# Kernel optimization log

Hardware: AMD Instinct MI355X
Metric: run time of the kernel (lower is better)

The kernel has to match this reference:

```python
import jax, jax.numpy as jnp
import numpy as np

D_MODEL = 512
N_HEADS = 8
HEAD_DIM = D_MODEL // N_HEADS
ROPE_BASE = 10000.0


def _rope_cache(seq_len, dtype):
    half = HEAD_DIM // 2
    inv_freq = 1.0 / (ROPE_BASE ** (jnp.arange(half, dtype=dtype) / half))
    t = jnp.arange(seq_len, dtype=dtype)
    freqs = jnp.einsum('i,j->ij', t, inv_freq)            # [L, half]
    cos = jnp.repeat(jnp.cos(freqs), 2, axis=-1)          # [L, head_dim]
    sin = jnp.repeat(jnp.sin(freqs), 2, axis=-1)
    return cos[None, None], sin[None, None]               # [1,1,L,head_dim]


def _rotate_half(x):
    x_even = x[..., ::2]
    x_odd = x[..., 1::2]
    return jnp.stack([-x_odd, x_even], axis=-1).reshape(x.shape)


def setup_inputs() -> dict:
    key = jax.random.key(0)
    ks = jax.random.split(key, 10)
    B, Lq, Lkv, C = 2, 2048, 4096, D_MODEL
    s = 1.0 / np.sqrt(C)
    inp = {
        'q': jax.random.normal(ks[0], (B, Lq, C), jnp.float32),
        'kv': jax.random.normal(ks[1], (B, Lkv, C), jnp.float32),
        'Wq': jax.random.normal(ks[2], (C, C), jnp.float32) * s,
        'bq': jnp.zeros((C,), jnp.float32),
        'Wk': jax.random.normal(ks[3], (C, C), jnp.float32) * s,
        'bk': jnp.zeros((C,), jnp.float32),
        'Wv': jax.random.normal(ks[4], (C, C), jnp.float32) * s,
        'bv': jnp.zeros((C,), jnp.float32),
        'Wo': jax.random.normal(ks[5], (C, C), jnp.float32) * s,
        'bo': jnp.zeros((C,), jnp.float32),
    }
    return inp


def reference(q, kv, Wq, bq, Wk, bk, Wv, bv, Wo, bo):
    B, Lq, C = q.shape
    Lkv = kv.shape[1]
    H, Dh = N_HEADS, HEAD_DIM
    # projections (torch Linear: x @ W.T + b)
    qh = (q @ Wq.T + bq).reshape(B, Lq, H, Dh).transpose(0, 2, 1, 3)    # [B,H,Lq,Dh]
    kh = (kv @ Wk.T + bk).reshape(B, Lkv, H, Dh).transpose(0, 2, 1, 3)  # [B,H,Lkv,Dh]
    vh = (kv @ Wv.T + bv).reshape(B, Lkv, H, Dh).transpose(0, 2, 1, 3)
    # RoPE applied to K only
    cos, sin = _rope_cache(Lkv, kh.dtype)
    kh = kh * cos + _rotate_half(kh) * sin
    # manual softmax attention (full [B,H,Lq,Lkv] matrix, as in the source)
    scale = 1.0 / np.sqrt(Dh).astype(np.float32)
    attn = jnp.einsum('bhqd,bhkd->bhqk', qh, kh) * scale
    attn = jax.nn.softmax(attn, axis=-1)
    out = jnp.einsum('bhqk,bhkd->bhqd', attn, vh)
    out = out.transpose(0, 2, 1, 3).reshape(B, Lq, C)
    return out @ Wo.T + bo
```

## Files before the change

kernel.cpp:

```cpp
#include <hip/hip_runtime.h>
#include <math.h>

typedef _Float16 f16;
typedef __attribute__((ext_vector_type(8))) f16 f16x8;
typedef __attribute__((ext_vector_type(2))) f16 f16x2;
typedef __attribute__((ext_vector_type(4))) float f32x4;
typedef __attribute__((ext_vector_type(4))) int   i32x4;

__device__ __forceinline__ short f2h(float f) {
    return __builtin_bit_cast(short, (f16)f);
}
__device__ __forceinline__ float h2f(short s) {
    return (float)__builtin_bit_cast(f16, s);
}

__device__ __forceinline__ void gload16(const void* g, void* l) {
    __builtin_amdgcn_global_load_lds(
        (const __attribute__((address_space(1))) unsigned int*)g,
        (__attribute__((address_space(3))) unsigned int*)l, 16, 0, 0);
}

#define MFMA16(A, B, C) __builtin_amdgcn_mfma_f32_16x16x32_f16(A, B, C, 0, 0, 0)

__global__ __launch_bounds__(256) void convert_kernel(
    const float* __restrict__ q, const float* __restrict__ kv,
    const float* __restrict__ Wq, const float* __restrict__ Wk,
    const float* __restrict__ Wv, const float* __restrict__ Wo,
    short* __restrict__ cq, short* __restrict__ ckv,
    short* __restrict__ wq, short* __restrict__ wk,
    short* __restrict__ wv, short* __restrict__ wo)
{
    int g = blockIdx.x * 256 + threadIdx.x;
    const float* src; short* dst; int local;
    if      (g <  524288) { src = q;  dst = cq;  local = g; }
    else if (g < 1572864) { src = kv; dst = ckv; local = g -  524288; }
    else if (g < 1638400) { src = Wq; dst = wq;  local = g - 1572864; }
    else if (g < 1703936) { src = Wk; dst = wk;  local = g - 1638400; }
    else if (g < 1769472) { src = Wv; dst = wv;  local = g - 1703936; }
    else                  { src = Wo; dst = wo;  local = g - 1769472; }
    float4 v = *(const float4*)(src + (size_t)local * 4);
    short4 hv; short* hp = (short*)&hv;
    hp[0] = f2h(v.x); hp[1] = f2h(v.y); hp[2] = f2h(v.z); hp[3] = f2h(v.w);
    *(short4*)(dst + (size_t)local * 4) = hv;
}

template<int RT, int EP>
__device__ __forceinline__ void gemm_core(
    short* As, short* Bs,
    const short* __restrict__ X, const short* __restrict__ W,
    const float* __restrict__ bias, float scale,
    float* __restrict__ outF, short* __restrict__ outH,
    int m0, int n0)
{
    const int tid  = threadIdx.x;
    const int wave = tid >> 6, lane = tid & 63;
    const int quad = lane >> 4, col = lane & 15;
    const int wy = wave >> 1, wx = wave & 1;
    constexpr int MT = RT / 32;

    f32x4 acc[MT][4];
    #pragma unroll
    for (int i = 0; i < MT; ++i)
        #pragma unroll
        for (int j = 0; j < 4; ++j) acc[i][j] = (f32x4){0.f, 0.f, 0.f, 0.f};

    int aoff[MT], boff[4];
    #pragma unroll
    for (int t = 0; t < MT; ++t)
        aoff[t] = (wy * (RT / 2) + t * 16 + col) * 32 + quad * 8;
    #pragma unroll
    for (int t = 0; t < 4; ++t)
        boff[t] = (wx * 64 + t * 16 + col) * 32 + quad * 8;

    const short* Abase = X + (size_t)m0 * 512;
    const short* Bbase = W + (size_t)n0 * 512;

    for (int kb = 0; kb < 512; kb += 32) {
        __syncthreads();
        #pragma unroll
        for (int i = 0; i < RT / 64; ++i) {
            int p = i * 256 + tid;
            int r = p >> 2, qq = p & 3;
            gload16(Abase + (size_t)r * 512 + kb + qq * 8,
                    &As[(i * 256 + wave * 64) * 8]);
        }
        #pragma unroll
        for (int i = 0; i < 2; ++i) {
            int p = i * 256 + tid;
            int r = p >> 2, qq = p & 3;
            gload16(Bbase + (size_t)r * 512 + kb + qq * 8,
                    &Bs[(i * 256 + wave * 64) * 8]);
        }
        __syncthreads();

        f16x8 a[MT], b[4];
        #pragma unroll
        for (int t = 0; t < MT; ++t) a[t] = *(const f16x8*)&As[aoff[t]];
        #pragma unroll
        for (int t = 0; t < 4; ++t)  b[t] = *(const f16x8*)&Bs[boff[t]];
        #pragma unroll
        for (int tm = 0; tm < MT; ++tm)
            #pragma unroll
            for (int tn = 0; tn < 4; ++tn)
                acc[tm][tn] = MFMA16(a[tm], b[tn], acc[tm][tn]);
    }

    #pragma unroll
    for (int tn = 0; tn < 4; ++tn) {
        int ng = n0 + wx * 64 + tn * 16 + col;
        float bb = bias[ng];
        #pragma unroll
        for (int tm = 0; tm < MT; ++tm) {
            int mb = m0 + wy * (RT / 2) + tm * 16 + quad * 4;
            if constexpr (EP == 2) {
                int bb_ = mb >> 12, kvg = mb & 4095;
                int tile = kvg >> 7, kv128 = kvg & 127;
                int t01 = (kv128 >> 6) & 1, sv = (kv128 >> 4) & 3, qd = (kv128 >> 2) & 3;
                int hh = ng >> 6, dd = ng & 63, dt = dd >> 4, d15 = dd & 15;
                size_t base = ((((size_t)((bb_ * 8 + hh) * 32 + tile) * 16)
                               + sv * 4 + dt) * 64 + qd * 16 + d15) * 8 + t01 * 4;
                short4 s4; short* sp = (short*)&s4;
                #pragma unroll
                for (int r = 0; r < 4; ++r) sp[r] = f2h(acc[tm][tn][r] + bb);
                *(short4*)&outH[base] = s4;
            } else if constexpr (EP == 1) {
                #pragma unroll
                for (int r = 0; r < 4; ++r)
                    outH[(size_t)(mb + r) * 512 + ng] =
                        f2h((acc[tm][tn][r] + bb) * scale);
            } else {
                #pragma unroll
                for (int r = 0; r < 4; ++r)
                    outF[(size_t)(mb + r) * 512 + ng] = acc[tm][tn][r] + bb;
            }
        }
    }
}

__global__ __launch_bounds__(256) void fused_qkv_gemm_kernel(
    const short* __restrict__ cq, const short* __restrict__ ckv,
    const short* __restrict__ wq, const short* __restrict__ wk,
    const short* __restrict__ wv,
    const float* __restrict__ bq, const float* __restrict__ bk,
    const float* __restrict__ bv, float qscale,
    short* __restrict__ Qh, short* __restrict__ Kh, short* __restrict__ Vf)
{
    __shared__ short As[128 * 32], Bs[128 * 32];
    int bi = blockIdx.x;
    if (bi < 128) {
        gemm_core<128, 1>(As, Bs, cq, wq, bq, qscale, nullptr, Qh,
                          (bi >> 2) * 128, (bi & 3) * 128);
    } else if (bi < 384) {
        bi -= 128;
        gemm_core<128, 1>(As, Bs, ckv, wk, bk, 1.0f, nullptr, Kh,
                          (bi >> 2) * 128, (bi & 3) * 128);
    } else {
        bi -= 384;
        gemm_core<128, 2>(As, Bs, ckv, wv, bv, 1.0f, nullptr, Vf,
                          (bi >> 2) * 128, (bi & 3) * 128);
    }
}

__global__ __launch_bounds__(256) void gemm_o_kernel(
    const short* __restrict__ X, const short* __restrict__ W,
    const float* __restrict__ bias, float* __restrict__ outF)
{
    __shared__ short As[64 * 32], Bs[128 * 32];
    gemm_core<64, 0>(As, Bs, X, W, bias, 1.0f, outF, nullptr,
                     (int)(blockIdx.x >> 2) * 64, (int)(blockIdx.x & 3) * 128);
}

__global__ __launch_bounds__(256) void rope_kernel(short* __restrict__ Kh)
{
    __shared__ float2 tbl[4][32];
    const int t = threadIdx.x;
    const int g = blockIdx.x * 256 + t;
    if (t < 128) {
        int p = t >> 5, i = t & 31;
        int pos = (blockIdx.x * 4 + p) & 4095;
        float fr = expf((float)i * -0.28782313662425576f);
        float sv, cv;
        sincosf((float)pos * fr, &sv, &cv);
        tbl[p][i] = make_float2(cv, sv);
    }
    __syncthreads();

    int row = g >> 6;
    int c8  = (g & 63) * 8;
    size_t off = (size_t)row * 512 + c8;
    f16x8 hv = *(const f16x8*)&Kh[off];
    float x[8];
    #pragma unroll
    for (int j = 0; j < 8; ++j) x[j] = (float)hv[j];
    const int rl = row & 3;
    const int ib = (c8 & 63) >> 1;
    #pragma unroll
    for (int p = 0; p < 4; ++p) {
        float2 cs = tbl[rl][ib + p];
        float e = x[2 * p], o = x[2 * p + 1];
        x[2 * p]     = e * cs.x - o * cs.y;
        x[2 * p + 1] = o * cs.x + e * cs.y;
    }
    #pragma unroll
    for (int j = 0; j < 8; ++j) hv[j] = (f16)x[j];
    *(f16x8*)&Kh[off] = hv;
}

__global__ __launch_bounds__(256, 2) void attn_mfma_kernel(
    const short* __restrict__ Qh, const short* __restrict__ Kh,
    const short* __restrict__ Vfrag, short* __restrict__ AO)
{
    __shared__ char smem[65536];

    const int tid  = threadIdx.x;
    const int wave = tid >> 6;
    const int lane = tid & 63;
    const int quad = lane >> 4;
    const int l15  = lane & 15;

    const int bh = blockIdx.x & 15;
    const int qt = blockIdx.x >> 4;
    const int b  = bh >> 3, h = bh & 7;
    const int qb = qt * 64;

    f16x8 qf[4][2];
    #pragma unroll
    for (int tq = 0; tq < 4; ++tq)
        #pragma unroll
        for (int c = 0; c < 2; ++c)
            qf[tq][c] = *(const f16x8*)&Qh[((size_t)(b * 2048 + qb + tq * 16 + l15)) * 512
                                           + h * 64 + c * 32 + quad * 8];

    f32x4 o[4][4];
    f32x4 l4[4];
    #pragma unroll
    for (int i = 0; i < 4; ++i) {
        l4[i] = (f32x4){0.f, 0.f, 0.f, 0.f};
        #pragma unroll
        for (int j = 0; j < 4; ++j) o[i][j] = (f32x4){0.f, 0.f, 0.f, 0.f};
    }

    f16x8 vones;
    #pragma unroll
    for (int j = 0; j < 8; ++j) vones[j] = (f16)1.0f;

    const short* kp = Kh + ((size_t)(b * 4096 + wave * 16 + l15)) * 512
                      + h * 64 + quad * 8;
    const short* vbase = Vfrag + (size_t)(b * 8 + h) * 262144
                         + ((size_t)(wave * 4) * 64 + lane) * 8;

    short* sw = (short*)smem + wave * 8192;

#define STG(I2, P) {                                                         \
    const short* _src = kp + (size_t)(I2) * 65536;                           \
    short* _dst = sw + (P) * 2048;                                           \
    gload16(_src,              _dst);                                        \
    gload16(_src + 32,         _dst + 512);                                  \
    gload16(_src + 32768,      _dst + 1024);                                 \
    gload16(_src + 32768 + 32, _dst + 1536);                                 \
}

    STG(0, 0); STG(1, 1);
    f16x8 vf0[4], vf1[4];
    #pragma unroll
    for (int dt = 0; dt < 4; ++dt) vf0[dt] = *(const f16x8*)(vbase + dt * 512);

#define AITER(I, PAR, NPAR, VCUR, VNXT) {                                    \
           \
    asm volatile("s_waitcnt vmcnt(8)" ::: "memory");                         \
    const short* kb = sw + (PAR) * 2048;                                     \
    f16x8 k0[2], k1[2];                                                      \
    k0[0] = *(const f16x8*)(kb + lane * 8);                                  \
    k0[1] = *(const f16x8*)(kb + 512 + lane * 8);                            \
    k1[0] = *(const f16x8*)(kb + 1024 + lane * 8);                           \
    k1[1] = *(const f16x8*)(kb + 1536 + lane * 8);                           \
    {   const short* _vn = vbase + (size_t)((I) + 1) * 8192;                 \
        _Pragma("unroll")                                                    \
        for (int dt = 0; dt < 4; ++dt)                                       \
            VNXT[dt] = *(const f16x8*)(_vn + dt * 512); }                    \
    STG((I) + 2, NPAR);                                                      \
    f32x4 s0[4], s1[4];                                                      \
    _Pragma("unroll")                                                        \
    for (int t = 0; t < 4; ++t) {                                            \
        s0[t] = (f32x4){0.f, 0.f, 0.f, 0.f};                                 \
        s1[t] = (f32x4){0.f, 0.f, 0.f, 0.f};                                 \
    }                                                                        \
    __builtin_amdgcn_s_setprio(1);                                           \
    _Pragma("unroll")                                                        \
    for (int c = 0; c < 2; ++c)                                              \
        _Pragma("unroll")                                                    \
        for (int t = 0; t < 4; ++t) {                                        \
            s0[t] = MFMA16(k0[c], qf[t][c], s0[t]);                          \
            s1[t] = MFMA16(k1[c], qf[t][c], s1[t]);                          \
        }                                                                    \
    __builtin_amdgcn_s_setprio(0);                                           \
    _Pragma("unroll")                                                        \
    for (int t = 0; t < 4; ++t) {                                            \
        float e0 = exp2f(s0[t][0]), e1 = exp2f(s0[t][1]);                    \
        float e2 = exp2f(s0[t][2]), e3 = exp2f(s0[t][3]);                    \
        float e4 = exp2f(s1[t][0]), e5 = exp2f(s1[t][1]);                    \
        float e6 = exp2f(s1[t][2]), e7 = exp2f(s1[t][3]);                    \
        i32x4 pw;                                                            \
        pw.x = __builtin_bit_cast(int, __builtin_amdgcn_cvt_pkrtz(e0, e1));  \
        pw.y = __builtin_bit_cast(int, __builtin_amdgcn_cvt_pkrtz(e2, e3));  \
        pw.z = __builtin_bit_cast(int, __builtin_amdgcn_cvt_pkrtz(e4, e5));  \
        pw.w = __builtin_bit_cast(int, __builtin_amdgcn_cvt_pkrtz(e6, e7));  \
        f16x8 p8 = __builtin_bit_cast(f16x8, pw);                            \
        __builtin_amdgcn_s_setprio(1);                                       \
        _Pragma("unroll")                                                    \
        for (int dt = 0; dt < 4; ++dt)                                       \
            o[t][dt] = MFMA16(p8, VCUR[dt], o[t][dt]);                       \
        l4[t] = MFMA16(p8, vones, l4[t]);                                    \
        __builtin_amdgcn_s_setprio(0);                                       \
    }                                                                        \
}

    #pragma unroll 1
    for (int j = 0; j < 32; j += 4) {
        AITER(j + 0, 0, 2, vf0, vf1);
        AITER(j + 1, 1, 3, vf1, vf0);
        AITER(j + 2, 2, 0, vf0, vf1);
        AITER(j + 3, 3, 1, vf1, vf0);
    }
#undef AITER
#undef STG

    asm volatile("s_waitcnt vmcnt(0)" ::: "memory");
    __syncthreads();
    float* Opart = (float*)smem;
    float* Lpart = (float*)(smem + 33792);

    float inv_save[8];
    #pragma unroll
    for (int pass = 0; pass < 2; ++pass) {
        if (pass) __syncthreads();
        #pragma unroll
        for (int tq = 0; tq < 4; ++tq)
            #pragma unroll
            for (int dh = 0; dh < 2; ++dh) {
                int dt = pass * 2 + dh;
                #pragma unroll
                for (int r = 0; r < 4; ++r)
                    Opart[wave * (64 * 33) + (tq * 16 + quad * 4 + r) * 33 + dh * 16 + l15] = o[tq][dt][r];
            }
        if (pass == 0 && l15 == 0) {
            #pragma unroll
            for (int tq = 0; tq < 4; ++tq)
                #pragma unroll
                for (int r = 0; r < 4; ++r)
                    Lpart[wave * 64 + tq * 16 + quad * 4 + r] = l4[tq][r];
        }
        __syncthreads();
        #pragma unroll
        for (int r = 0; r < 8; ++r) {
            int qq = wave * 16 + r * 2 + (lane >> 5);
            int d  = lane & 31;
            float v = Opart[0 * (64 * 33) + qq * 33 + d] + Opart[1 * (64 * 33) + qq * 33 + d]
                    + Opart[2 * (64 * 33) + qq * 33 + d] + Opart[3 * (64 * 33) + qq * 33 + d];
            float inv;
            if (pass == 0) {
                float l = Lpart[qq] + Lpart[64 + qq] + Lpart[128 + qq] + Lpart[192 + qq];
                inv = 1.0f / l;
                inv_save[r] = inv;
            } else {
                inv = inv_save[r];
            }
            float val = v * inv;
            size_t oo = ((size_t)(b * 2048 + qb + qq)) * 512 + h * 64 + pass * 32 + d;
            AO[oo] = f2h(val);
        }
    }
}

extern "C" void kernel_launch(void* const* d_in, const int* in_sizes, int n_in,
                              void* d_out, int out_size, void* d_ws, size_t ws_size,
                              hipStream_t stream) {
    const float* q  = (const float*)d_in[0];
    const float* kv = (const float*)d_in[1];
    const float* Wq = (const float*)d_in[2];
    const float* bq = (const float*)d_in[3];
    const float* Wk = (const float*)d_in[4];
    const float* bk = (const float*)d_in[5];
    const float* Wv = (const float*)d_in[6];
    const float* bv = (const float*)d_in[7];
    const float* Wo = (const float*)d_in[8];
    const float* bo = (const float*)d_in[9];
    float* out = (float*)d_out;

    char* ws = (char*)d_ws;
    const size_t MB = 1024 * 1024;
    short* cq  = (short*)(ws + 0 * MB);
    short* ckv = (short*)(ws + 4 * MB);
    short* wq  = (short*)(ws + 12 * MB);
    short* wk  = wq + 262144;
    short* wv  = wk + 262144;
    short* wo  = wv + 262144;
    short* Qh  = (short*)(ws + 14 * MB);
    short* Kh  = (short*)(ws + 18 * MB);
    short* Vf  = (short*)(ws + 26 * MB);
    short* AO  = (short*)(ws + 34 * MB);

    const float qscale = 0.18033688011112043f;

    dim3 blk(256);
    convert_kernel<<<7168, blk, 0, stream>>>(
        q, kv, Wq, Wk, Wv, Wo, cq, ckv, wq, wk, wv, wo);

    fused_qkv_gemm_kernel<<<640, blk, 0, stream>>>(
        cq, ckv, wq, wk, wv, bq, bk, bv, qscale, Qh, Kh, Vf);

    rope_kernel<<<2048, blk, 0, stream>>>(Kh);

    attn_mfma_kernel<<<512, blk, 0, stream>>>(Qh, Kh, Vf, AO);

    gemm_o_kernel<<<256, blk, 0, stream>>>(AO, wo, bo, out);
}
```

Before: 175.7 us.

## Double-buffer GEMM LDS tiles and software-pipeline attention loop with register K/V

Result: faster. 166.1 us (-5.5%).

```diff
diff --git a/kernel.cpp b/kernel.cpp
--- a/kernel.cpp
+++ b/kernel.cpp
@@ -3,7 +3,6 @@
 
 typedef _Float16 f16;
 typedef __attribute__((ext_vector_type(8))) f16 f16x8;
-typedef __attribute__((ext_vector_type(2))) f16 f16x2;
 typedef __attribute__((ext_vector_type(4))) float f32x4;
 typedef __attribute__((ext_vector_type(4))) int   i32x4;
 
@@ -21,6 +20,7 @@
 }
 
 #define MFMA16(A, B, C) __builtin_amdgcn_mfma_f32_16x16x32_f16(A, B, C, 0, 0, 0)
+#define EXP2(x) __builtin_amdgcn_exp2f(x)
 
 __global__ __launch_bounds__(256) void convert_kernel(
     const float* __restrict__ q, const float* __restrict__ kv,
@@ -56,7 +56,8 @@
     const int wave = tid >> 6, lane = tid & 63;
     const int quad = lane >> 4, col = lane & 15;
     const int wy = wave >> 1, wx = wave & 1;
-    constexpr int MT = RT / 32;
+    constexpr int MT  = RT / 32;
+    constexpr int ASZ = RT * 32;
 
     f32x4 acc[MT][4];
     #pragma unroll
@@ -75,35 +76,42 @@
     const short* Abase = X + (size_t)m0 * 512;
     const short* Bbase = W + (size_t)n0 * 512;
 
+#define STAGE_G(BUF, KB) {                                                   \
+    _Pragma("unroll")                                                        \
+    for (int i = 0; i < RT / 64; ++i) {                                      \
+        int p = i * 256 + tid; int r = p >> 2, qq = p & 3;                   \
+        gload16(Abase + (size_t)r * 512 + (KB) + qq * 8,                     \
+                &As[(BUF) * ASZ + (i * 256 + wave * 64) * 8]);               \
+    }                                                                        \
+    _Pragma("unroll")                                                        \
+    for (int i = 0; i < 2; ++i) {                                            \
+        int p = i * 256 + tid; int r = p >> 2, qq = p & 3;                   \
+        gload16(Bbase + (size_t)r * 512 + (KB) + qq * 8,                     \
+                &Bs[(BUF) * 4096 + (i * 256 + wave * 64) * 8]);              \
+    }                                                                        \
+}
+
+    STAGE_G(0, 0);
+    asm volatile("s_waitcnt vmcnt(0)" ::: "memory");
+    __syncthreads();
+
     for (int kb = 0; kb < 512; kb += 32) {
-        __syncthreads();
-        #pragma unroll
-        for (int i = 0; i < RT / 64; ++i) {
-            int p = i * 256 + tid;
-            int r = p >> 2, qq = p & 3;
-            gload16(Abase + (size_t)r * 512 + kb + qq * 8,
-                    &As[(i * 256 + wave * 64) * 8]);
-        }
-        #pragma unroll
-        for (int i = 0; i < 2; ++i) {
-            int p = i * 256 + tid;
-            int r = p >> 2, qq = p & 3;
-            gload16(Bbase + (size_t)r * 512 + kb + qq * 8,
-                    &Bs[(i * 256 + wave * 64) * 8]);
-        }
-        __syncthreads();
-
+        const int cur = (kb >> 5) & 1;
+        if (kb + 32 < 512) STAGE_G(cur ^ 1, kb + 32);
         f16x8 a[MT], b[4];
         #pragma unroll
-        for (int t = 0; t < MT; ++t) a[t] = *(const f16x8*)&As[aoff[t]];
-        #pragma unroll
-        for (int t = 0; t < 4; ++t)  b[t] = *(const f16x8*)&Bs[boff[t]];
+        for (int t = 0; t < MT; ++t) a[t] = *(const f16x8*)&As[cur * ASZ + aoff[t]];
+        #pragma unroll
+        for (int t = 0; t < 4; ++t)  b[t] = *(const f16x8*)&Bs[cur * 4096 + boff[t]];
         #pragma unroll
         for (int tm = 0; tm < MT; ++tm)
             #pragma unroll
             for (int tn = 0; tn < 4; ++tn)
                 acc[tm][tn] = MFMA16(a[tm], b[tn], acc[tm][tn]);
-    }
+        asm volatile("s_waitcnt vmcnt(0)" ::: "memory");
+        __syncthreads();
+    }
+#undef STAGE_G
 
     #pragma unroll
     for (int tn = 0; tn < 4; ++tn) {
@@ -145,7 +153,7 @@
     const float* __restrict__ bv, float qscale,
     short* __restrict__ Qh, short* __restrict__ Kh, short* __restrict__ Vf)
 {
-    __shared__ short As[128 * 32], Bs[128 * 32];
+    __shared__ short As[2 * 128 * 32], Bs[2 * 128 * 32];
     int bi = blockIdx.x;
     if (bi < 128) {
         gemm_core<128, 1>(As, Bs, cq, wq, bq, qscale, nullptr, Qh,
@@ -165,7 +173,7 @@
     const short* __restrict__ X, const short* __restrict__ W,
     const float* __restrict__ bias, float* __restrict__ outF)
 {
-    __shared__ short As[64 * 32], Bs[128 * 32];
+    __shared__ short As[2 * 64 * 32], Bs[2 * 128 * 32];
     gemm_core<64, 0>(As, Bs, X, W, bias, 1.0f, outF, nullptr,
                      (int)(blockIdx.x >> 2) * 64, (int)(blockIdx.x & 3) * 128);
 }
@@ -210,7 +218,7 @@
     const short* __restrict__ Qh, const short* __restrict__ Kh,
     const short* __restrict__ Vfrag, short* __restrict__ AO)
 {
-    __shared__ char smem[65536];
+    __shared__ char smem[34816];
 
     const int tid  = threadIdx.x;
     const int wave = tid >> 6;
@@ -240,6 +248,7 @@
         for (int j = 0; j < 4; ++j) o[i][j] = (f32x4){0.f, 0.f, 0.f, 0.f};
     }
 
+    const f32x4 zero4 = (f32x4){0.f, 0.f, 0.f, 0.f};
     f16x8 vones;
     #pragma unroll
     for (int j = 0; j < 8; ++j) vones[j] = (f16)1.0f;
@@ -249,57 +258,35 @@
     const short* vbase = Vfrag + (size_t)(b * 8 + h) * 262144
                          + ((size_t)(wave * 4) * 64 + lane) * 8;
 
-    short* sw = (short*)smem + wave * 8192;
-
-#define STG(I2, P) {                                                         \
-    const short* _src = kp + (size_t)(I2) * 65536;                           \
-    short* _dst = sw + (P) * 2048;                                           \
-    gload16(_src,              _dst);                                        \
-    gload16(_src + 32,         _dst + 512);                                  \
-    gload16(_src + 32768,      _dst + 1024);                                 \
-    gload16(_src + 32768 + 32, _dst + 1536);                                 \
-}
-
-    STG(0, 0); STG(1, 1);
-    f16x8 vf0[4], vf1[4];
-    #pragma unroll
-    for (int dt = 0; dt < 4; ++dt) vf0[dt] = *(const f16x8*)(vbase + dt * 512);
-
-#define AITER(I, PAR, NPAR, VCUR, VNXT) {                                    \
-           \
-    asm volatile("s_waitcnt vmcnt(8)" ::: "memory");                         \
-    const short* kb = sw + (PAR) * 2048;                                     \
-    f16x8 k0[2], k1[2];                                                      \
-    k0[0] = *(const f16x8*)(kb + lane * 8);                                  \
-    k0[1] = *(const f16x8*)(kb + 512 + lane * 8);                            \
-    k1[0] = *(const f16x8*)(kb + 1024 + lane * 8);                           \
-    k1[1] = *(const f16x8*)(kb + 1536 + lane * 8);                           \
-    {   const short* _vn = vbase + (size_t)((I) + 1) * 8192;                 \
-        _Pragma("unroll")                                                    \
-        for (int dt = 0; dt < 4; ++dt)                                       \
-            VNXT[dt] = *(const f16x8*)(_vn + dt * 512); }                    \
-    STG((I) + 2, NPAR);                                                      \
-    f32x4 s0[4], s1[4];                                                      \
+#define LDK(DST, I) { const short* _k = kp + (size_t)(I) * 65536;            \
+    DST[0] = *(const f16x8*)(_k);                                            \
+    DST[1] = *(const f16x8*)(_k + 32);                                       \
+    DST[2] = *(const f16x8*)(_k + 32768);                                    \
+    DST[3] = *(const f16x8*)(_k + 32800); }
+#define LDV(DST, I) { const short* _v = vbase + (size_t)(I) * 8192;          \
+    DST[0] = *(const f16x8*)(_v);                                            \
+    DST[1] = *(const f16x8*)(_v + 512);                                      \
+    DST[2] = *(const f16x8*)(_v + 1024);                                     \
+    DST[3] = *(const f16x8*)(_v + 1536); }
+
+#define QK(KC) {                                                             \
+    __builtin_amdgcn_s_setprio(1);                                           \
     _Pragma("unroll")                                                        \
     for (int t = 0; t < 4; ++t) {                                            \
-        s0[t] = (f32x4){0.f, 0.f, 0.f, 0.f};                                 \
-        s1[t] = (f32x4){0.f, 0.f, 0.f, 0.f};                                 \
+        s0[t] = MFMA16(KC[0], qf[t][0], zero4);                              \
+        s0[t] = MFMA16(KC[1], qf[t][1], s0[t]);                              \
+        s1[t] = MFMA16(KC[2], qf[t][0], zero4);                              \
+        s1[t] = MFMA16(KC[3], qf[t][1], s1[t]);                              \
     }                                                                        \
-    __builtin_amdgcn_s_setprio(1);                                           \
-    _Pragma("unroll")                                                        \
-    for (int c = 0; c < 2; ++c)                                              \
-        _Pragma("unroll")                                                    \
-        for (int t = 0; t < 4; ++t) {                                        \
-            s0[t] = MFMA16(k0[c], qf[t][c], s0[t]);                          \
-            s1[t] = MFMA16(k1[c], qf[t][c], s1[t]);                          \
-        }                                                                    \
-    __builtin_amdgcn_s_setprio(0);                                           \
+    __builtin_amdgcn_s_setprio(0); }
+
+#define FIN(VP) {                                                            \
     _Pragma("unroll")                                                        \
     for (int t = 0; t < 4; ++t) {                                            \
-        float e0 = exp2f(s0[t][0]), e1 = exp2f(s0[t][1]);                    \
-        float e2 = exp2f(s0[t][2]), e3 = exp2f(s0[t][3]);                    \
-        float e4 = exp2f(s1[t][0]), e5 = exp2f(s1[t][1]);                    \
-        float e6 = exp2f(s1[t][2]), e7 = exp2f(s1[t][3]);                    \
+        float e0 = EXP2(s0[t][0]), e1 = EXP2(s0[t][1]);                      \
+        float e2 = EXP2(s0[t][2]), e3 = EXP2(s0[t][3]);                      \
+        float e4 = EXP2(s1[t][0]), e5 = EXP2(s1[t][1]);                      \
+        float e6 = EXP2(s1[t][2]), e7 = EXP2(s1[t][3]);                      \
         i32x4 pw;                                                            \
         pw.x = __builtin_bit_cast(int, __builtin_amdgcn_cvt_pkrtz(e0, e1));  \
         pw.y = __builtin_bit_cast(int, __builtin_amdgcn_cvt_pkrtz(e2, e3));  \
@@ -309,24 +296,37 @@
         __builtin_amdgcn_s_setprio(1);                                       \
         _Pragma("unroll")                                                    \
         for (int dt = 0; dt < 4; ++dt)                                       \
-            o[t][dt] = MFMA16(p8, VCUR[dt], o[t][dt]);                       \
+            o[t][dt] = MFMA16(p8, VP[dt], o[t][dt]);                         \
         l4[t] = MFMA16(p8, vones, l4[t]);                                    \
         __builtin_amdgcn_s_setprio(0);                                       \
-    }                                                                        \
-}
+    } }
+
+#define BODY(I, KC, KN, VP) {                                                \
+    LDK(KN, (I) + 1);                                                        \
+    FIN(VP);                                                                 \
+    LDV(VP, (I) + 1);                                                        \
+    QK(KC); }
+
+    f16x8 kA[4], kB[4], vA[4], vB[4];
+    f32x4 s0[4], s1[4];
+
+    LDK(kA, 0); LDV(vA, 0); LDK(kB, 1); LDV(vB, 1);
+    QK(kA);
 
     #pragma unroll 1
-    for (int j = 0; j < 32; j += 4) {
-        AITER(j + 0, 0, 2, vf0, vf1);
-        AITER(j + 1, 1, 3, vf1, vf0);
-        AITER(j + 2, 2, 0, vf0, vf1);
-        AITER(j + 3, 3, 1, vf1, vf0);
-    }
-#undef AITER
-#undef STG
-
-    asm volatile("s_waitcnt vmcnt(0)" ::: "memory");
-    __syncthreads();
+    for (int j = 1; j < 31; j += 2) {
+        BODY(j,     kB, kA, vA);
+        BODY(j + 1, kA, kB, vB);
+    }
+    BODY(31, kB, kA, vA);
+    FIN(vB);
+
+#undef BODY
+#undef FIN
+#undef QK
+#undef LDV
+#undef LDK
+
     float* Opart = (float*)smem;
     float* Lpart = (float*)(smem + 33792);
 
```
